# Kernel optimization log

Measured on AMD Instinct MI355X. Metric: run time of the kernel, lower is better.

The kernel has to match this reference:

```python
import jax, jax.numpy as jnp
import numpy as np
from jax import lax

B, T, I, H, O = 128, 512, 256, 512, 256


def setup_inputs() -> dict:
    key = jax.random.key(0)
    ks = jax.random.split(key, 7)
    s_ih = 1.0 / np.sqrt(H)
    return {
        "inputs": jax.random.normal(ks[0], (B, T, I), dtype=jnp.float32),
        "W_ih": jax.random.uniform(ks[1], (H, I), jnp.float32, -s_ih, s_ih),
        "b_ih": jax.random.uniform(ks[2], (H,), jnp.float32, -s_ih, s_ih),
        "W_hh": jax.random.uniform(ks[3], (H, H), jnp.float32, -s_ih, s_ih),
        "b_hh": jax.random.uniform(ks[4], (H,), jnp.float32, -s_ih, s_ih),
        "W_out": jax.random.uniform(ks[5], (O, H), jnp.float32, -s_ih, s_ih),
        "b_out": jax.random.uniform(ks[6], (O,), jnp.float32, -s_ih, s_ih),
        "h0": jnp.zeros((H,), dtype=jnp.float32),
    }


def reference(inputs, W_ih, b_ih, W_hh, b_hh, W_out, b_out, h0):
    # inputs: [B, T, I]; returns readout of last hidden state: [B, O]
    Bsz, Tlen = inputs.shape[0], inputs.shape[1]
    inv_T = jnp.asarray(1.0 / Tlen, dtype=inputs.dtype)
    # Precompute input projection for all timesteps (one big GEMM):
    # x_proj[b,t,h] = inputs @ W_ih.T + b_ih + b_hh
    x_proj = jnp.einsum('bti,hi->bth', inputs, W_ih) + (b_ih + b_hh)
    x_proj_t = jnp.swapaxes(x_proj, 0, 1)  # [T, B, H]

    def step(h, xp):
        # RNNCell: tanh(xp + h @ W_hh.T); residual scaling by 1/T
        h_new = jnp.tanh(xp + h @ W_hh.T) * inv_T + h
        return h_new, None

    h_init = jnp.broadcast_to(h0, (Bsz, h0.shape[0]))
    h_last, _ = lax.scan(step, h_init, x_proj_t)
    return h_last @ W_out.T + b_out
```

## Files before the change

### kernel.cpp

```cpp
#include <hip/hip_runtime.h>
#include <stdint.h>

#define NB 128
#define NT 512
#define NI 256
#define NH 512
#define NO 256

__device__ __forceinline__ uint16_t f2bf(float x) {
  uint32_t u = __float_as_uint(x);
  return (uint16_t)((u + 0x7fffu + ((u >> 16) & 1u)) >> 16);
}
__device__ __forceinline__ uint32_t pack2bf(float a, float b) {
  return (uint32_t)f2bf(a) | ((uint32_t)f2bf(b) << 16);
}

__device__ __forceinline__ float fast_tanh(float x) {
  float e = __expf(2.0f * x);
#if __has_builtin(__builtin_amdgcn_rcpf)
  return 1.0f - 2.0f * __builtin_amdgcn_rcpf(e + 1.0f);
#else
  return 1.0f - 2.0f / (e + 1.0f);
#endif
}

typedef __bf16 bf16x8 __attribute__((ext_vector_type(8)));
typedef float f32x4 __attribute__((ext_vector_type(4)));

__device__ __forceinline__ f32x4 mfma16(bf16x8 a, uint4 b, f32x4 c) {
  return __builtin_amdgcn_mfma_f32_16x16x32_bf16(a, __builtin_bit_cast(bf16x8, b), c, 0, 0, 0);
}
__device__ __forceinline__ f32x4 mfma16_ab(uint4 a, bf16x8 b, f32x4 c) {
  return __builtin_amdgcn_mfma_f32_16x16x32_bf16(__builtin_bit_cast(bf16x8, a), b, c, 0, 0, 0);
}

__global__ __launch_bounds__(256) void prep_kernel(const float* __restrict__ Whh,
                                                   const float* __restrict__ Wih,
                                                   const float* __restrict__ Wout,
                                                   const float* __restrict__ bih,
                                                   const float* __restrict__ bhh,
                                                   uint4* __restrict__ WB,
                                                   float* __restrict__ WoT,
                                                   uint4* __restrict__ WihF,
                                                   float* __restrict__ BS) {
  int idx = blockIdx.x * 256 + threadIdx.x;
  if (idx < 32768) {
    int q = idx >> 9, t = idx & 511;
    int u = q >> 4, tk = q & 15;
    int n = (t >> 6) * 64 + u * 16 + (t & 15);
    int kb = tk * 32 + ((t >> 4) & 3) * 8;
    const float* row = Whh + (size_t)n * NH + kb;
    float4 f0 = *(const float4*)row;
    float4 f1 = *(const float4*)(row + 4);
    uint4 wq;
    wq.x = pack2bf(f0.x, f0.y);
    wq.y = pack2bf(f0.z, f0.w);
    wq.z = pack2bf(f1.x, f1.y);
    wq.w = pack2bf(f1.z, f1.w);
    WB[idx] = wq;
  } else if (idx < 49152) {
    int i = idx - 32768;
    int l = i & 63;
    int uk = i >> 6;
    int k0 = uk & 7, u = uk >> 3;
    int n = u * 16 + (l & 15);
    int kb = k0 * 32 + (l >> 4) * 8;
    const float* row = Wih + (size_t)n * NI + kb;
    float4 f0 = *(const float4*)row;
    float4 f1 = *(const float4*)(row + 4);
    uint4 wq;
    wq.x = pack2bf(f0.x, f0.y);
    wq.y = pack2bf(f0.z, f0.w);
    wq.z = pack2bf(f1.x, f1.y);
    wq.w = pack2bf(f1.z, f1.w);
    WihF[i] = wq;
  } else if (idx < 81920) {
    int i = idx - 49152;
    int o4 = (i & 63) * 4;
    int k = i >> 6;
    float4 v;
    v.x = Wout[(size_t)(o4 + 0) * NH + k];
    v.y = Wout[(size_t)(o4 + 1) * NH + k];
    v.z = Wout[(size_t)(o4 + 2) * NH + k];
    v.w = Wout[(size_t)(o4 + 3) * NH + k];
    *(float4*)&WoT[(size_t)k * NO + o4] = v;
  } else if (idx < 82432) {
    int n = idx - 81920;
    BS[n] = bih[n] + bhh[n];
  }
}

__device__ __forceinline__ void ld_pack(uint4 (&af)[8], const float* __restrict__ A,
                                        int mt, int sl, int quad) {
  const float* ar = A + (size_t)(mt * 16 + sl) * NI + quad * 8;
#pragma unroll
  for (int k0 = 0; k0 < 8; ++k0) {
    float4 f0 = *(const float4*)(ar + k0 * 32);
    float4 f1 = *(const float4*)(ar + k0 * 32 + 4);
    uint4 ap;
    ap.x = pack2bf(f0.x, f0.y);
    ap.y = pack2bf(f0.z, f0.w);
    ap.z = pack2bf(f1.x, f1.y);
    ap.w = pack2bf(f1.z, f1.w);
    af[k0] = ap;
  }
}

__device__ __forceinline__ void do_tile(const uint4 (&af)[8], const uint4 (&Wb)[32],
                                        const float4 (&bs)[4], uint16_t* __restrict__ XP,
                                        int g, int mt, int sl, int quad) {
  f32x4 acc[4] = {};
#pragma unroll
  for (int k0 = 0; k0 < 8; ++k0) {
    bf16x8 a = __builtin_bit_cast(bf16x8, af[k0]);
#pragma unroll
    for (int u = 0; u < 4; ++u) acc[u] = mfma16_ab(Wb[u * 8 + k0], a, acc[u]);
  }
  uint16_t* xrow = XP + (size_t)(mt * 16 + sl) * NH + g * 64 + quad * 4;
#pragma unroll
  for (int u = 0; u < 4; ++u) {
    uint2 pw;
    pw.x = pack2bf(acc[u][0] + bs[u].x, acc[u][1] + bs[u].y);
    pw.y = pack2bf(acc[u][2] + bs[u].z, acc[u][3] + bs[u].w);
    *(uint2*)(xrow + u * 16) = pw;
  }
}

__global__ __launch_bounds__(256, 2) void xproj_kernel(const float* __restrict__ A,
                                                       const uint4* __restrict__ WihF,
                                                       const float* __restrict__ BS,
                                                       uint16_t* __restrict__ XP) {
  const int w = threadIdx.x >> 6;
  const int l = threadIdx.x & 63;
  const int sl = l & 15, quad = l >> 4;
  const int g = blockIdx.y;
  const int mt0 = blockIdx.x * 16 + w * 4;

  uint4 Wb[32];
#pragma unroll
  for (int u = 0; u < 4; ++u)
#pragma unroll
    for (int k0 = 0; k0 < 8; ++k0)
      Wb[u * 8 + k0] = WihF[(size_t)((g * 4 + u) * 8 + k0) * 64 + l];

  float4 bs[4];
#pragma unroll
  for (int u = 0; u < 4; ++u) bs[u] = *(const float4*)(BS + (g * 4 + u) * 16 + quad * 4);

  uint4 afA[8], afB[8];
  ld_pack(afA, A, mt0 + 0, sl, quad);
  ld_pack(afB, A, mt0 + 1, sl, quad);
  do_tile(afA, Wb, bs, XP, g, mt0 + 0, sl, quad);
  ld_pack(afA, A, mt0 + 2, sl, quad);
  do_tile(afB, Wb, bs, XP, g, mt0 + 1, sl, quad);
  ld_pack(afB, A, mt0 + 3, sl, quad);
  do_tile(afA, Wb, bs, XP, g, mt0 + 2, sl, quad);
  do_tile(afB, Wb, bs, XP, g, mt0 + 3, sl, quad);
}

__global__ __launch_bounds__(512, 2) void recur_kernel(const uint4* __restrict__ WB,
                                                       const float* __restrict__ WoT,
                                                       const uint16_t* __restrict__ XP,
                                                       const float* __restrict__ h0,
                                                       const float* __restrict__ bout,
                                                       float* __restrict__ out) {
  __shared__ uint4 WL[12][512];
  __shared__ __align__(16) uint16_t h2[2][NH];
  __shared__ float hsf[NH];
  const int t = threadIdx.x;
  const int b = blockIdx.x;
  const int w = t >> 6;
  const int sl = t & 15, quad = (t >> 4) & 3;
  const int myn = w * 64 + quad * 16 + sl;
  const float invT = 1.0f / (float)NT;

  uint4 Wr[52];
#pragma unroll
  for (int q = 0; q < 52; ++q) Wr[q] = WB[q * 512 + t];
#pragma unroll
  for (int i = 0; i < 12; ++i) WL[i][t] = WB[(52 + i) * 512 + t];

  float hj = h0[myn];
  h2[0][myn] = f2bf(hj);
  __syncthreads();

  const uint16_t* xpb = XP + (size_t)b * NT * NH + myn;
  uint16_t xpr = xpb[0];

  for (int ts = 0; ts < NT; ++ts) {
    const int cur = ts & 1;
    const int nts = (ts + 1 < NT) ? (ts + 1) : (NT - 1);
    uint16_t xpn = xpb[(size_t)nts * NH];

    const uint16_t* hbuf = h2[cur];
    f32x4 acc0 = {}, acc1 = {}, acc2 = {}, acc3 = {};
#pragma unroll
    for (int tk = 0; tk < 16; ++tk) {
      bf16x8 hfrag = *(const bf16x8*)(hbuf + tk * 32 + quad * 8);
      acc0 = mfma16(hfrag, Wr[tk], acc0);
      acc1 = mfma16(hfrag, Wr[16 + tk], acc1);
      acc2 = mfma16(hfrag, Wr[32 + tk], acc2);
      uint4 w3 = (tk < 4) ? Wr[48 + tk] : WL[tk - 4][t];
      acc3 = mfma16(hfrag, w3, acc3);
    }
    float y = (quad == 0) ? acc0[0] : (quad == 1) ? acc1[0] : (quad == 2) ? acc2[0] : acc3[0];
    float xpj = __uint_as_float((uint32_t)xpr << 16);
    float hnew = fmaf(fast_tanh(xpj + y), invT, hj);
    hj = hnew;
    h2[cur ^ 1][myn] = f2bf(hnew);
    xpr = xpn;
    __syncthreads();
  }

  hsf[myn] = hj;
  __syncthreads();

  if (t < NO) {
    float c0 = 0.f, c1 = 0.f;
#pragma unroll 4
    for (int k = 0; k < NH; k += 2) {
      c0 = fmaf(WoT[(size_t)k * NO + t], hsf[k], c0);
      c1 = fmaf(WoT[(size_t)(k + 1) * NO + t], hsf[k + 1], c1);
    }
    out[(size_t)b * NO + t] = c0 + c1 + bout[t];
  }
}

extern "C" void kernel_launch(void* const* d_in, const int* in_sizes, int n_in,
                              void* d_out, int out_size, void* d_ws, size_t ws_size,
                              hipStream_t stream) {
  const float* inputs = (const float*)d_in[0];
  const float* Wih    = (const float*)d_in[1];
  const float* bih    = (const float*)d_in[2];
  const float* Whh    = (const float*)d_in[3];
  const float* bhh    = (const float*)d_in[4];
  const float* Wout   = (const float*)d_in[5];
  const float* bout   = (const float*)d_in[6];
  const float* h0     = (const float*)d_in[7];
  float* out = (float*)d_out;

  char* ws = (char*)d_ws;
  uint4*    WB   = (uint4*)ws;
  float*    WoT  = (float*)(ws + (512u << 10));
  uint4*    WihF = (uint4*)(ws + (1024u << 10));
  float*    BS   = (float*)(ws + (1280u << 10));
  uint16_t* XP   = (uint16_t*)(ws + (1536u << 10));

  hipLaunchKernelGGL(prep_kernel, dim3(322), dim3(256), 0, stream,
                     Whh, Wih, Wout, bih, bhh, WB, WoT, WihF, BS);
  hipLaunchKernelGGL(xproj_kernel, dim3(NB * NT / 256, 8), dim3(256), 0, stream,
                     inputs, WihF, BS, XP);
  hipLaunchKernelGGL(recur_kernel, dim3(NB), dim3(512), 0, stream,
                     WB, WoT, XP, h0, bout, out);
}
```

Measured before the change: 872.6 us.

## Restructure xproj to load input tiles once and stream weight slices

The input projection kernel previously launched an 8-way grid over output column groups, so each block reloaded and re-packed the fp32 input rows 8 times while keeping 32 weight fragments in registers. Now each wave loads and packs two 16-row input tiles once and loops over all 32 weight column slices, double-buffering weight fragment loads from global memory. This cuts redundant reads and bf16 conversion of the large input tensor. In exchange, weight fragments are re-read per wave (they are small and likely cache-resident), the grid shrinks to 512 blocks, and the loop is serialized over column slices.

```diff
diff --git a/kernel.cpp b/kernel.cpp
--- a/kernel.cpp
+++ b/kernel.cpp
@@ -106,24 +106,35 @@
   }
 }
 
-__device__ __forceinline__ void do_tile(const uint4 (&af)[8], const uint4 (&Wb)[32],
-                                        const float4 (&bs)[4], uint16_t* __restrict__ XP,
-                                        int g, int mt, int sl, int quad) {
-  f32x4 acc[4] = {};
+__device__ __forceinline__ void ld_w(uint4 (&Wc)[8], float4& bsv,
+                                     const uint4* __restrict__ WihF,
+                                     const float* __restrict__ BS,
+                                     int gu, int l, int quad) {
+  const int U = gu >> 2 << 2 | (gu & 3);
+#pragma unroll
+  for (int k0 = 0; k0 < 8; ++k0) Wc[k0] = WihF[(size_t)(gu * 8 + k0) * 64 + l];
+  bsv = *(const float4*)(BS + U * 16 + quad * 4);
+}
+
+__device__ __forceinline__ void do_gu(const uint4 (&Wc)[8], const float4 bsv,
+                                      const uint4 (&afA)[8], const uint4 (&afB)[8],
+                                      uint16_t* __restrict__ XP,
+                                      int gu, int mt0, int sl, int quad) {
+  const int g = gu >> 2, u = gu & 3;
+  f32x4 a0 = {}, a1 = {};
 #pragma unroll
   for (int k0 = 0; k0 < 8; ++k0) {
-    bf16x8 a = __builtin_bit_cast(bf16x8, af[k0]);
-#pragma unroll
-    for (int u = 0; u < 4; ++u) acc[u] = mfma16_ab(Wb[u * 8 + k0], a, acc[u]);
-  }
-  uint16_t* xrow = XP + (size_t)(mt * 16 + sl) * NH + g * 64 + quad * 4;
-#pragma unroll
-  for (int u = 0; u < 4; ++u) {
-    uint2 pw;
-    pw.x = pack2bf(acc[u][0] + bs[u].x, acc[u][1] + bs[u].y);
-    pw.y = pack2bf(acc[u][2] + bs[u].z, acc[u][3] + bs[u].w);
-    *(uint2*)(xrow + u * 16) = pw;
-  }
+    a0 = mfma16_ab(Wc[k0], __builtin_bit_cast(bf16x8, afA[k0]), a0);
+    a1 = mfma16_ab(Wc[k0], __builtin_bit_cast(bf16x8, afB[k0]), a1);
+  }
+  const size_t col = (size_t)(g * 64 + quad * 4 + u * 16);
+  uint2 p0, p1;
+  p0.x = pack2bf(a0[0] + bsv.x, a0[1] + bsv.y);
+  p0.y = pack2bf(a0[2] + bsv.z, a0[3] + bsv.w);
+  p1.x = pack2bf(a1[0] + bsv.x, a1[1] + bsv.y);
+  p1.y = pack2bf(a1[2] + bsv.z, a1[3] + bsv.w);
+  *(uint2*)(XP + (size_t)(mt0 * 16 + sl) * NH + col) = p0;
+  *(uint2*)(XP + (size_t)((mt0 + 1) * 16 + sl) * NH + col) = p1;
 }
 
 __global__ __launch_bounds__(256, 2) void xproj_kernel(const float* __restrict__ A,
@@ -133,29 +144,22 @@
   const int w = threadIdx.x >> 6;
   const int l = threadIdx.x & 63;
   const int sl = l & 15, quad = l >> 4;
-  const int g = blockIdx.y;
-  const int mt0 = blockIdx.x * 16 + w * 4;
-
-  uint4 Wb[32];
-#pragma unroll
-  for (int u = 0; u < 4; ++u)
-#pragma unroll
-    for (int k0 = 0; k0 < 8; ++k0)
-      Wb[u * 8 + k0] = WihF[(size_t)((g * 4 + u) * 8 + k0) * 64 + l];
-
-  float4 bs[4];
-#pragma unroll
-  for (int u = 0; u < 4; ++u) bs[u] = *(const float4*)(BS + (g * 4 + u) * 16 + quad * 4);
+  const int mt0 = blockIdx.x * 8 + w * 2;
 
   uint4 afA[8], afB[8];
   ld_pack(afA, A, mt0 + 0, sl, quad);
   ld_pack(afB, A, mt0 + 1, sl, quad);
-  do_tile(afA, Wb, bs, XP, g, mt0 + 0, sl, quad);
-  ld_pack(afA, A, mt0 + 2, sl, quad);
-  do_tile(afB, Wb, bs, XP, g, mt0 + 1, sl, quad);
-  ld_pack(afB, A, mt0 + 3, sl, quad);
-  do_tile(afA, Wb, bs, XP, g, mt0 + 2, sl, quad);
-  do_tile(afB, Wb, bs, XP, g, mt0 + 3, sl, quad);
+
+  uint4 WcA[8], WcB[8];
+  float4 bsA, bsB;
+  ld_w(WcA, bsA, WihF, BS, 0, l, quad);
+#pragma unroll 1
+  for (int gu = 0; gu < 32; gu += 2) {
+    ld_w(WcB, bsB, WihF, BS, gu + 1, l, quad);
+    do_gu(WcA, bsA, afA, afB, XP, gu, mt0, sl, quad);
+    if (gu + 2 < 32) ld_w(WcA, bsA, WihF, BS, gu + 2, l, quad);
+    do_gu(WcB, bsB, afA, afB, XP, gu + 1, mt0, sl, quad);
+  }
 }
 
 __global__ __launch_bounds__(512, 2) void recur_kernel(const uint4* __restrict__ WB,
@@ -248,7 +252,7 @@
 
   hipLaunchKernelGGL(prep_kernel, dim3(322), dim3(256), 0, stream,
                      Whh, Wih, Wout, bih, bhh, WB, WoT, WihF, BS);
-  hipLaunchKernelGGL(xproj_kernel, dim3(NB * NT / 256, 8), dim3(256), 0, stream,
+  hipLaunchKernelGGL(xproj_kernel, dim3(512), dim3(256), 0, stream,
                      inputs, WihF, BS, XP);
   hipLaunchKernelGGL(recur_kernel, dim3(NB), dim3(512), 0, stream,
                      WB, WoT, XP, h0, bout, out);
```

New measurement: 827.4 us. 5.2% less time.
